# Kernel optimization log

Measured on AMD Instinct MI355X. Metric: run time of the kernel, lower is better.

## Reference

```python
import jax, jax.numpy as jnp
import numpy as np

B, T, U, D, V = 8, 128, 64, 512, 1024

def setup_inputs() -> dict:
    key = jax.random.key(0)
    k1, k2, k3, k4, k5, k6 = jax.random.split(key, 6)
    source_encodings = jax.random.normal(k1, (B, T, D), dtype=jnp.float32)
    target_encodings = jax.random.normal(k2, (B, U, D), dtype=jnp.float32)
    source_lengths = jax.random.randint(k3, (B,), 1, T + 1, dtype=jnp.int32)
    target_lengths = jax.random.randint(k4, (B,), 1, U + 1, dtype=jnp.int32)
    # Linear(D, V): weight (V, D), bias (V), init like torch default (uniform)
    bound = 1.0 / np.sqrt(D)
    W = jax.random.uniform(k5, (V, D), minval=-bound, maxval=bound, dtype=jnp.float32)
    b = jax.random.uniform(k6, (V,), minval=-bound, maxval=bound, dtype=jnp.float32)
    return {"source_encodings": source_encodings, "source_lengths": source_lengths,
            "target_encodings": target_encodings, "target_lengths": target_lengths,
            "W": W, "b": b}

def reference(source_encodings, source_lengths, target_encodings, target_lengths, W, b):
    # broadcast add: (B,T,1,D) + (B,1,U,D) -> (B,T,U,D)
    joint = source_encodings[:, :, None, :] + target_encodings[:, None, :, :]
    relu_out = jax.nn.relu(joint)
    # linear projection: (B,T,U,D) x (D,V) + b -> (B,T,U,V)
    output = jnp.einsum('btud,vd->btuv', relu_out, W) + b
    return (output, source_lengths, target_lengths)
```

## Files before the change

### kernel.cpp

```cpp
#include <hip/hip_runtime.h>

typedef unsigned short u16;
typedef float  f32x4  __attribute__((ext_vector_type(4)));
typedef int    i32x4  __attribute__((ext_vector_type(4)));
typedef __bf16 bf16x8 __attribute__((ext_vector_type(8)));

#define AS1 __attribute__((address_space(1)))
#define AS3 __attribute__((address_space(3)))

constexpr int B_ = 8, T_ = 128, U_ = 64, D_ = 512, V_ = 1024;
constexpr int M_ = B_ * T_ * U_;

__global__ void prep_w(const float* __restrict__ W,
                       const int* __restrict__ sl, const int* __restrict__ tl,
                       u16* __restrict__ Wb2, float* __restrict__ tail) {
  if (blockIdx.x == 0 && threadIdx.x < 16) {
    const int t = threadIdx.x;
    tail[t] = (t < 8) ? (float)sl[t] : (float)tl[t - 8];
  }
  const int tid = blockIdx.x * 256 + threadIdx.x;
  const int v  = tid >> 6;
  const int cs = tid & 63;
  const float* sp = W + (size_t)v * D_ + cs * 8;
  float4 w0 = *(const float4*)sp;
  float4 w1 = *(const float4*)(sp + 4);
  union { __bf16 h[8]; i32x4 x; } pk;
  pk.h[0] = (__bf16)w0.x; pk.h[1] = (__bf16)w0.y;
  pk.h[2] = (__bf16)w0.z; pk.h[3] = (__bf16)w0.w;
  pk.h[4] = (__bf16)w1.x; pk.h[5] = (__bf16)w1.y;
  pk.h[6] = (__bf16)w1.z; pk.h[7] = (__bf16)w1.w;
  const int vg = v >> 4, vc = v & 15;
  const int kc = cs >> 2, ko = cs & 3;
  *(i32x4*)(Wb2 + (((size_t)(vg * 16 + kc) * 64 + ko * 16 + vc) * 8)) = pk.x;
}

__global__ void tail_k(const int* __restrict__ sl, const int* __restrict__ tl,
                       float* __restrict__ tail) {
  const int t = threadIdx.x;
  if (t < 8)       tail[t] = (float)sl[t];
  else if (t < 16) tail[t] = (float)tl[t - 8];
}

__global__ __launch_bounds__(256, 3) void joiner_gemm(
    const float* __restrict__ src, const float* __restrict__ tgt,
    const u16* __restrict__ Wb2, const float* __restrict__ bias,
    float* __restrict__ out)
{
  __shared__ __align__(16) char As[16384];

  const int tid  = threadIdx.x;
  const int lane = tid & 63;
  const int wid  = tid >> 6;
  const int bn   = blockIdx.x & 7;
  const int bm   = blockIdx.x >> 3;
  const int bt0  = bm * 2;
  const int bb   = bt0 >> 7;
  const int sr0  = tid >> 3;
  const int sc8  = tid & 7;
  const int wm   = (wid >> 1) * 64;
  const int wn   = (wid & 1) * 64;

  f32x4 acc[4][4] = {};

  const float* srcp0 = src + (size_t)bt0 * D_ + sc8 * 8;
  const float* srcp1 = srcp0 + D_;
  const float* tgtp0 = tgt + ((size_t)bb * U_ + sr0) * D_ + sc8 * 8;
  const float* tgtp1 = tgtp0 + (size_t)32 * D_;

  float bv[4];
  #pragma unroll
  for (int ni = 0; ni < 4; ++ni)
    bv[ni] = bias[bn * 128 + wn + ni * 16 + (lane & 15)];

  const u16* bfr[4];
  #pragma unroll
  for (int ni = 0; ni < 4; ++ni) {
    const int vg = bn * 8 + (wn >> 4) + ni;
    bfr[ni] = Wb2 + ((size_t)vg * 16 * 64 + lane) * 8;
  }

  float4 pS0a, pS0b, pS1a, pS1b, pT0a, pT0b, pT1a, pT1b;
  bf16x8 bg[4][2];

  auto loadA = [&](int kt) {
    const int k0 = kt * 64;
    pS0a = *(const float4*)(srcp0 + k0); pS0b = *(const float4*)(srcp0 + k0 + 4);
    pS1a = *(const float4*)(srcp1 + k0); pS1b = *(const float4*)(srcp1 + k0 + 4);
    pT0a = *(const float4*)(tgtp0 + k0); pT0b = *(const float4*)(tgtp0 + k0 + 4);
    pT1a = *(const float4*)(tgtp1 + k0); pT1b = *(const float4*)(tgtp1 + k0 + 4);
  };

  auto loadBg = [&](int kt) {
    #pragma unroll
    for (int ni = 0; ni < 4; ++ni)
      #pragma unroll
      for (int s = 0; s < 2; ++s)
        bg[ni][s] = *(const bf16x8*)(bfr[ni] + (size_t)(kt * 2 + s) * 512);
  };

  auto expandA = [&]() {
    #pragma unroll
    for (int i = 0; i < 2; ++i) {
      const float4 sa = i ? pS1a : pS0a;
      const float4 sb = i ? pS1b : pS0b;
      #pragma unroll
      for (int j = 0; j < 2; ++j) {
        const float4 ta = j ? pT1a : pT0a;
        const float4 tb = j ? pT1b : pT0b;
        const int r = i * 64 + j * 32 + sr0;
        union { __bf16 h[8]; i32x4 x; } pk;
        pk.h[0] = (__bf16)fmaxf(sa.x + ta.x, 0.f);
        pk.h[1] = (__bf16)fmaxf(sa.y + ta.y, 0.f);
        pk.h[2] = (__bf16)fmaxf(sa.z + ta.z, 0.f);
        pk.h[3] = (__bf16)fmaxf(sa.w + ta.w, 0.f);
        pk.h[4] = (__bf16)fmaxf(sb.x + tb.x, 0.f);
        pk.h[5] = (__bf16)fmaxf(sb.y + tb.y, 0.f);
        pk.h[6] = (__bf16)fmaxf(sb.z + tb.z, 0.f);
        pk.h[7] = (__bf16)fmaxf(sb.w + tb.w, 0.f);
        *(i32x4*)(As + r * 128 + ((sc8 ^ (r & 7)) << 4)) = pk.x;
      }
    }
  };

  auto compute = [&]() {
    #pragma unroll
    for (int s = 0; s < 2; ++s) {
      const int kc = s * 4 + (lane >> 4);
      bf16x8 af[4];
      #pragma unroll
      for (int mi = 0; mi < 4; ++mi) {
        const int r = wm + mi * 16 + (lane & 15);
        af[mi] = *(const bf16x8*)(As + r * 128 + ((kc ^ (r & 7)) << 4));
      }
      __builtin_amdgcn_s_setprio(1);
      #pragma unroll
      for (int mi = 0; mi < 4; ++mi)
        #pragma unroll
        for (int ni = 0; ni < 4; ++ni)
          acc[mi][ni] = __builtin_amdgcn_mfma_f32_16x16x32_bf16(
              af[mi], bg[ni][s], acc[mi][ni], 0, 0, 0);
      __builtin_amdgcn_s_setprio(0);
    }
  };

  loadA(0);
  expandA();
  loadBg(0);
  asm volatile("s_waitcnt lgkmcnt(0)" ::: "memory");
  __builtin_amdgcn_sched_barrier(0);
  __builtin_amdgcn_s_barrier();
  __builtin_amdgcn_sched_barrier(0);

  for (int kt = 0; kt < 8; ++kt) {
    if (kt < 7) loadA(kt + 1);
    __builtin_amdgcn_sched_barrier(0);
    compute();
    __builtin_amdgcn_sched_barrier(0);
    __builtin_amdgcn_s_barrier();
    __builtin_amdgcn_sched_barrier(0);
    if (kt < 7) {
      loadBg(kt + 1);
      expandA();
      asm volatile("s_waitcnt lgkmcnt(0)" ::: "memory");
      __builtin_amdgcn_sched_barrier(0);
      __builtin_amdgcn_s_barrier();
      __builtin_amdgcn_sched_barrier(0);
    }
  }

  const int col = lane & 15;
  const int r4  = (lane >> 4) * 4;
  #pragma unroll
  for (int mi = 0; mi < 4; ++mi) {
    const size_t mrow = (size_t)bm * 128 + wm + mi * 16 + r4;
    float* op0 = out + mrow * V_ + bn * 128 + wn + col;
    #pragma unroll
    for (int ni = 0; ni < 4; ++ni) {
      float* op = op0 + ni * 16;
      const f32x4 v = acc[mi][ni];
      op[0 * V_] = v[0] + bv[ni];
      op[1 * V_] = v[1] + bv[ni];
      op[2 * V_] = v[2] + bv[ni];
      op[3 * V_] = v[3] + bv[ni];
    }
  }
}

__global__ __launch_bounds__(256, 2) void joiner_gemm_f32(
    const float* __restrict__ src, const float* __restrict__ tgt,
    const float* __restrict__ Wf, const float* __restrict__ bias,
    float* __restrict__ out)
{
  __shared__ char As[128 * 128];
  __shared__ char Bs[128 * 128];

  const int tid  = threadIdx.x;
  const int lane = tid & 63;
  const int wid  = tid >> 6;
  const int bn   = blockIdx.x & 7;
  const int bm   = blockIdx.x >> 3;
  const int bt0  = bm * 2;
  const int bb   = bt0 >> 7;
  const int sr0  = tid >> 3;
  const int sc8  = tid & 7;
  const int wm   = (wid >> 1) * 64;
  const int wn   = (wid & 1) * 64;

  f32x4 acc[4][4] = {};

  const float* srcp0 = src + (size_t)bt0 * D_ + sc8 * 8;
  const float* srcp1 = srcp0 + D_;
  const float* tgtp0 = tgt + ((size_t)bb * U_ + sr0) * D_ + sc8 * 8;
  const float* tgtp1 = tgtp0 + (size_t)32 * D_;

  for (int kt = 0; kt < 8; ++kt) {
    const int k0 = kt * 64;
    #pragma unroll
    for (int jj = 0; jj < 4; ++jj) {
      const int vr = sr0 + 32 * jj;
      const float* wp = Wf + (size_t)(bn * 128 + vr) * D_ + k0 + sc8 * 8;
      float4 w0 = *(const float4*)wp;
      float4 w1 = *(const float4*)(wp + 4);
      union { __bf16 h[8]; i32x4 x; } pk;
      pk.h[0] = (__bf16)w0.x; pk.h[1] = (__bf16)w0.y;
      pk.h[2] = (__bf16)w0.z; pk.h[3] = (__bf16)w0.w;
      pk.h[4] = (__bf16)w1.x; pk.h[5] = (__bf16)w1.y;
      pk.h[6] = (__bf16)w1.z; pk.h[7] = (__bf16)w1.w;
      *(i32x4*)(Bs + vr * 128 + ((sc8 ^ (vr & 7)) << 4)) = pk.x;
    }
    float4 s0a = *(const float4*)(srcp0 + k0), s0b = *(const float4*)(srcp0 + k0 + 4);
    float4 s1a = *(const float4*)(srcp1 + k0), s1b = *(const float4*)(srcp1 + k0 + 4);
    float4 t0a = *(const float4*)(tgtp0 + k0), t0b = *(const float4*)(tgtp0 + k0 + 4);
    float4 t1a = *(const float4*)(tgtp1 + k0), t1b = *(const float4*)(tgtp1 + k0 + 4);
    #pragma unroll
    for (int i = 0; i < 2; ++i) {
      const float4 sa = i ? s1a : s0a;
      const float4 sb = i ? s1b : s0b;
      #pragma unroll
      for (int jj = 0; jj < 2; ++jj) {
        const float4 ta = jj ? t1a : t0a;
        const float4 tb = jj ? t1b : t0b;
        const int r = i * 64 + jj * 32 + sr0;
        union { __bf16 h[8]; i32x4 x; } pk;
        pk.h[0] = (__bf16)fmaxf(sa.x + ta.x, 0.f);
        pk.h[1] = (__bf16)fmaxf(sa.y + ta.y, 0.f);
        pk.h[2] = (__bf16)fmaxf(sa.z + ta.z, 0.f);
        pk.h[3] = (__bf16)fmaxf(sa.w + ta.w, 0.f);
        pk.h[4] = (__bf16)fmaxf(sb.x + tb.x, 0.f);
        pk.h[5] = (__bf16)fmaxf(sb.y + tb.y, 0.f);
        pk.h[6] = (__bf16)fmaxf(sb.z + tb.z, 0.f);
        pk.h[7] = (__bf16)fmaxf(sb.w + tb.w, 0.f);
        *(i32x4*)(As + r * 128 + ((sc8 ^ (r & 7)) << 4)) = pk.x;
      }
    }
    __syncthreads();
    #pragma unroll
    for (int s = 0; s < 2; ++s) {
      const int kc = s * 4 + (lane >> 4);
      bf16x8 af[4], bg[4];
      #pragma unroll
      for (int mi = 0; mi < 4; ++mi) {
        const int r = wm + mi * 16 + (lane & 15);
        af[mi] = *(const bf16x8*)(As + r * 128 + ((kc ^ (r & 7)) << 4));
      }
      #pragma unroll
      for (int ni = 0; ni < 4; ++ni) {
        const int n = wn + ni * 16 + (lane & 15);
        bg[ni] = *(const bf16x8*)(Bs + n * 128 + ((kc ^ (n & 7)) << 4));
      }
      #pragma unroll
      for (int mi = 0; mi < 4; ++mi)
        #pragma unroll
        for (int ni = 0; ni < 4; ++ni)
          acc[mi][ni] = __builtin_amdgcn_mfma_f32_16x16x32_bf16(
              af[mi], bg[ni], acc[mi][ni], 0, 0, 0);
    }
    __syncthreads();
  }

  const int col = lane & 15;
  const int r4  = (lane >> 4) * 4;
  float bv[4];
  #pragma unroll
  for (int ni = 0; ni < 4; ++ni) bv[ni] = bias[bn * 128 + wn + ni * 16 + col];
  #pragma unroll
  for (int mi = 0; mi < 4; ++mi) {
    const size_t mrow = (size_t)bm * 128 + wm + mi * 16 + r4;
    float* op0 = out + mrow * V_ + bn * 128 + wn + col;
    #pragma unroll
    for (int ni = 0; ni < 4; ++ni) {
      float* op = op0 + ni * 16;
      const f32x4 v = acc[mi][ni];
      op[0 * V_] = v[0] + bv[ni];
      op[1 * V_] = v[1] + bv[ni];
      op[2 * V_] = v[2] + bv[ni];
      op[3 * V_] = v[3] + bv[ni];
    }
  }
}

extern "C" void kernel_launch(void* const* d_in, const int* in_sizes, int n_in,
                              void* d_out, int out_size, void* d_ws, size_t ws_size,
                              hipStream_t stream) {
  const float* src  = (const float*)d_in[0];
  const int*   sl   = (const int*)d_in[1];
  const float* tgt  = (const float*)d_in[2];
  const int*   tl   = (const int*)d_in[3];
  const float* W    = (const float*)d_in[4];
  const float* bias = (const float*)d_in[5];
  float* out  = (float*)d_out;
  float* tail = out + (size_t)M_ * V_;

  if (ws_size >= (size_t)V_ * D_ * sizeof(u16)) {
    u16* Wb2 = (u16*)d_ws;
    prep_w<<<256, 256, 0, stream>>>(W, sl, tl, Wb2, tail);
    joiner_gemm<<<(M_ / 128) * (V_ / 128), 256, 0, stream>>>(
        src, tgt, Wb2, bias, out);
  } else {
    tail_k<<<1, 64, 0, stream>>>(sl, tl, tail);
    joiner_gemm_f32<<<(M_ / 128) * (V_ / 128), 256, 0, stream>>>(
        src, tgt, W, bias, out);
  }
}
```

Baseline: 103.4 us.

## Give each wave a private 64x64 tile to drop block barriers

Restructures the fused GEMM so each wave owns one (b,t) row group of 64 U-rows and a 64-wide V slice, with a private LDS buffer. This removes all block-level barriers and the register prefetch of A. Bias is folded into the accumulator initialisation, and block IDs are remapped so consecutive blocks share the same W slice. In exchange, each wave reloads W fragments for a smaller tile, which raises B traffic per FLOP. Loads are no longer overlapped with compute through explicit prefetch.

```diff
diff --git a/kernel.cpp b/kernel.cpp
--- a/kernel.cpp
+++ b/kernel.cpp
@@ -4,9 +4,6 @@
 typedef float  f32x4  __attribute__((ext_vector_type(4)));
 typedef int    i32x4  __attribute__((ext_vector_type(4)));
 typedef __bf16 bf16x8 __attribute__((ext_vector_type(8)));
-
-#define AS1 __attribute__((address_space(1)))
-#define AS3 __attribute__((address_space(3)))
 
 constexpr int B_ = 8, T_ = 128, U_ = 64, D_ = 512, V_ = 1024;
 constexpr int M_ = B_ * T_ * U_;
@@ -46,49 +43,41 @@
     const u16* __restrict__ Wb2, const float* __restrict__ bias,
     float* __restrict__ out)
 {
-  __shared__ __align__(16) char As[16384];
+  __shared__ __align__(16) char As[4][8192];
 
   const int tid  = threadIdx.x;
   const int lane = tid & 63;
   const int wid  = tid >> 6;
-  const int bn   = blockIdx.x & 7;
-  const int bm   = blockIdx.x >> 3;
-  const int bt0  = bm * 2;
-  const int bb   = bt0 >> 7;
-  const int sr0  = tid >> 3;
-  const int sc8  = tid & 7;
-  const int wm   = (wid >> 1) * 64;
-  const int wn   = (wid & 1) * 64;
-
-  f32x4 acc[4][4] = {};
-
-  const float* srcp0 = src + (size_t)bt0 * D_ + sc8 * 8;
-  const float* srcp1 = srcp0 + D_;
-  const float* tgtp0 = tgt + ((size_t)bb * U_ + sr0) * D_ + sc8 * 8;
-  const float* tgtp1 = tgtp0 + (size_t)32 * D_;
-
-  float bv[4];
+  const int id   = blockIdx.x;
+  const int nid  = (id & 7) * 512 + (id >> 3);
+  const int bn   = nid >> 8;
+  const int btg  = nid & 255;
+  const int bt   = btg * 4 + wid;
+  const int b    = bt >> 7;
+  char* A = As[wid];
+
+  const int cl  = lane & 15;
+  const int kl  = lane >> 4;
+  const int sr0 = lane >> 3;
+  const int sc8 = lane & 7;
+
+  f32x4 acc[4][4];
+  #pragma unroll
+  for (int ni = 0; ni < 4; ++ni) {
+    const float bv = bias[bn * 64 + ni * 16 + cl];
+    #pragma unroll
+    for (int mi = 0; mi < 4; ++mi) acc[mi][ni] = f32x4{bv, bv, bv, bv};
+  }
+
+  const float* srcp = src + (size_t)bt * D_ + sc8 * 8;
+  const float* tgtp = tgt + ((size_t)b * U_ + sr0) * D_ + sc8 * 8;
+
+  const u16* bfr[4];
   #pragma unroll
   for (int ni = 0; ni < 4; ++ni)
-    bv[ni] = bias[bn * 128 + wn + ni * 16 + (lane & 15)];
-
-  const u16* bfr[4];
-  #pragma unroll
-  for (int ni = 0; ni < 4; ++ni) {
-    const int vg = bn * 8 + (wn >> 4) + ni;
-    bfr[ni] = Wb2 + ((size_t)vg * 16 * 64 + lane) * 8;
-  }
-
-  float4 pS0a, pS0b, pS1a, pS1b, pT0a, pT0b, pT1a, pT1b;
+    bfr[ni] = Wb2 + ((size_t)(bn * 4 + ni) * 16 * 64 + lane) * 8;
+
   bf16x8 bg[4][2];
-
-  auto loadA = [&](int kt) {
-    const int k0 = kt * 64;
-    pS0a = *(const float4*)(srcp0 + k0); pS0b = *(const float4*)(srcp0 + k0 + 4);
-    pS1a = *(const float4*)(srcp1 + k0); pS1b = *(const float4*)(srcp1 + k0 + 4);
-    pT0a = *(const float4*)(tgtp0 + k0); pT0b = *(const float4*)(tgtp0 + k0 + 4);
-    pT1a = *(const float4*)(tgtp1 + k0); pT1b = *(const float4*)(tgtp1 + k0 + 4);
-  };
 
   auto loadBg = [&](int kt) {
     #pragma unroll
@@ -98,39 +87,38 @@
         bg[ni][s] = *(const bf16x8*)(bfr[ni] + (size_t)(kt * 2 + s) * 512);
   };
 
-  auto expandA = [&]() {
-    #pragma unroll
-    for (int i = 0; i < 2; ++i) {
-      const float4 sa = i ? pS1a : pS0a;
-      const float4 sb = i ? pS1b : pS0b;
-      #pragma unroll
-      for (int j = 0; j < 2; ++j) {
-        const float4 ta = j ? pT1a : pT0a;
-        const float4 tb = j ? pT1b : pT0b;
-        const int r = i * 64 + j * 32 + sr0;
-        union { __bf16 h[8]; i32x4 x; } pk;
-        pk.h[0] = (__bf16)fmaxf(sa.x + ta.x, 0.f);
-        pk.h[1] = (__bf16)fmaxf(sa.y + ta.y, 0.f);
-        pk.h[2] = (__bf16)fmaxf(sa.z + ta.z, 0.f);
-        pk.h[3] = (__bf16)fmaxf(sa.w + ta.w, 0.f);
-        pk.h[4] = (__bf16)fmaxf(sb.x + tb.x, 0.f);
-        pk.h[5] = (__bf16)fmaxf(sb.y + tb.y, 0.f);
-        pk.h[6] = (__bf16)fmaxf(sb.z + tb.z, 0.f);
-        pk.h[7] = (__bf16)fmaxf(sb.w + tb.w, 0.f);
-        *(i32x4*)(As + r * 128 + ((sc8 ^ (r & 7)) << 4)) = pk.x;
-      }
+  auto stageA = [&](int kt) {
+    const int k0 = kt * 64;
+    const float4 sa = *(const float4*)(srcp + k0);
+    const float4 sb = *(const float4*)(srcp + k0 + 4);
+    #pragma unroll
+    for (int i = 0; i < 8; ++i) {
+      const float* tp = tgtp + (size_t)(8 * i) * D_ + k0;
+      const float4 ta = *(const float4*)tp;
+      const float4 tb = *(const float4*)(tp + 4);
+      const int r = sr0 + 8 * i;
+      union { __bf16 h[8]; i32x4 x; } pk;
+      pk.h[0] = (__bf16)fmaxf(sa.x + ta.x, 0.f);
+      pk.h[1] = (__bf16)fmaxf(sa.y + ta.y, 0.f);
+      pk.h[2] = (__bf16)fmaxf(sa.z + ta.z, 0.f);
+      pk.h[3] = (__bf16)fmaxf(sa.w + ta.w, 0.f);
+      pk.h[4] = (__bf16)fmaxf(sb.x + tb.x, 0.f);
+      pk.h[5] = (__bf16)fmaxf(sb.y + tb.y, 0.f);
+      pk.h[6] = (__bf16)fmaxf(sb.z + tb.z, 0.f);
+      pk.h[7] = (__bf16)fmaxf(sb.w + tb.w, 0.f);
+      *(i32x4*)(A + r * 128 + ((sc8 ^ (r & 7)) << 4)) = pk.x;
     }
   };
 
   auto compute = [&]() {
     #pragma unroll
     for (int s = 0; s < 2; ++s) {
-      const int kc = s * 4 + (lane >> 4);
+      const int kc = s * 4 + kl;
       bf16x8 af[4];
       #pragma unroll
       for (int mi = 0; mi < 4; ++mi) {
-        const int r = wm + mi * 16 + (lane & 15);
-        af[mi] = *(const bf16x8*)(As + r * 128 + ((kc ^ (r & 7)) << 4));
+        const int r = mi * 16 + cl;
+        af[mi] = *(const bf16x8*)(A + r * 128 + ((kc ^ (r & 7)) << 4));
       }
       __builtin_amdgcn_s_setprio(1);
       #pragma unroll
@@ -143,45 +131,27 @@
     }
   };
 
-  loadA(0);
-  expandA();
   loadBg(0);
-  asm volatile("s_waitcnt lgkmcnt(0)" ::: "memory");
-  __builtin_amdgcn_sched_barrier(0);
-  __builtin_amdgcn_s_barrier();
-  __builtin_amdgcn_sched_barrier(0);
-
+  stageA(0);
+  #pragma unroll
   for (int kt = 0; kt < 8; ++kt) {
-    if (kt < 7) loadA(kt + 1);
-    __builtin_amdgcn_sched_barrier(0);
     compute();
-    __builtin_amdgcn_sched_barrier(0);
-    __builtin_amdgcn_s_barrier();
-    __builtin_amdgcn_sched_barrier(0);
-    if (kt < 7) {
-      loadBg(kt + 1);
-      expandA();
-      asm volatile("s_waitcnt lgkmcnt(0)" ::: "memory");
-      __builtin_amdgcn_sched_barrier(0);
-      __builtin_amdgcn_s_barrier();
-      __builtin_amdgcn_sched_barrier(0);
-    }
-  }
-
-  const int col = lane & 15;
-  const int r4  = (lane >> 4) * 4;
+    if (kt < 7) { loadBg(kt + 1); stageA(kt + 1); }
+  }
+
+  const int r4 = kl * 4;
   #pragma unroll
   for (int mi = 0; mi < 4; ++mi) {
-    const size_t mrow = (size_t)bm * 128 + wm + mi * 16 + r4;
-    float* op0 = out + mrow * V_ + bn * 128 + wn + col;
+    const size_t mrow = (size_t)bt * U_ + mi * 16 + r4;
+    float* op0 = out + mrow * V_ + bn * 64 + cl;
     #pragma unroll
     for (int ni = 0; ni < 4; ++ni) {
       float* op = op0 + ni * 16;
       const f32x4 v = acc[mi][ni];
-      op[0 * V_] = v[0] + bv[ni];
-      op[1 * V_] = v[1] + bv[ni];
-      op[2 * V_] = v[2] + bv[ni];
-      op[3 * V_] = v[3] + bv[ni];
+      op[0 * V_] = v[0];
+      op[1 * V_] = v[1];
+      op[2 * V_] = v[2];
+      op[3 * V_] = v[3];
     }
   }
 }
@@ -314,8 +284,7 @@
   if (ws_size >= (size_t)V_ * D_ * sizeof(u16)) {
     u16* Wb2 = (u16*)d_ws;
     prep_w<<<256, 256, 0, stream>>>(W, sl, tl, Wb2, tail);
-    joiner_gemm<<<(M_ / 128) * (V_ / 128), 256, 0, stream>>>(
-        src, tgt, Wb2, bias, out);
+    joiner_gemm<<<4096, 256, 0, stream>>>(src, tgt, Wb2, bias, out);
   } else {
     tail_k<<<1, 64, 0, stream>>>(sl, tl, tail);
     joiner_gemm_f32<<<(M_ / 128) * (V_ / 128), 256, 0, stream>>>(
```

Result: slower. 166.9 us (+61.4%).
